# Kernel optimization log

Hardware: AMD Instinct MI355X
Metric: run time of the kernel (lower is better)

## Reference

```python
import jax, jax.numpy as jnp
import numpy as np


def _propagate(x, src, dst, norm, n):
    # PyG propagate with aggr='add': out[dst_e] += norm_e * x[src_e]
    return jax.ops.segment_sum(x[src] * norm[:, None], dst, num_segments=n)


def _dconv(x, w, b, row, col, norm_out, norm_in, n):
    # DConv with K=2: w has shape (2, 2, c_in, c_out)
    # k=0 term: identity for both diffusion directions
    h = x @ w[0, 0] + x @ w[1, 0]
    # k=1 term: 1-hop diffusion, forward edges and flipped edges
    tx_o = _propagate(x, row, col, norm_out, n)  # out-degree normalized walk
    tx_i = _propagate(x, col, row, norm_in, n)   # edge_index.flip([0]) walk
    h = h + tx_o @ w[0, 1] + tx_i @ w[1, 1]
    return h + b


def reference(x, edge_index, edge_weight, w_lin2, b_lin2, w_z, b_z, w_r, b_r, w_h, b_h, w_out, b_out):
    n = x.shape[0]
    row, col = edge_index[0], edge_index[1]
    # degrees from weighted adjacency (same as to_dense_adj row/col sums)
    deg_out = jax.ops.segment_sum(edge_weight, row, num_segments=n)
    deg_in = jax.ops.segment_sum(edge_weight, col, num_segments=n)
    norm_out = (1.0 / deg_out)[row]
    norm_in = (1.0 / deg_in)[row]

    h = x.reshape(n, -1)                      # Flatten: (n, 24)
    h = jax.nn.sigmoid(h @ w_lin2 + b_lin2)   # (n, hidden)

    # DCRNN GRU cell, hidden state initialized to zeros (single step)
    h0 = jnp.zeros_like(h)
    xh = jnp.concatenate([h, h0], axis=1)     # (n, 2*hidden)
    z = jax.nn.sigmoid(_dconv(xh, w_z, b_z, row, col, norm_out, norm_in, n))
    r = jax.nn.sigmoid(_dconv(xh, w_r, b_r, row, col, norm_out, norm_in, n))
    xhr = jnp.concatenate([h, h0 * r], axis=1)
    h_tilde = jnp.tanh(_dconv(xhr, w_h, b_h, row, col, norm_out, norm_in, n))
    h_new = z * h0 + (1.0 - z) * h_tilde

    return jax.nn.sigmoid(h_new) @ w_out + b_out  # (n, out_periods)


def setup_inputs() -> dict:
    key = jax.random.key(0)
    ks = jax.random.split(key, 12)
    N, DEG, HID, OUTP, WIN, HOR = 100000, 8, 64, 12, 2, 12
    E = N * DEG

    x = jax.random.normal(ks[0], (N, WIN, HOR), dtype=jnp.float32)

    # random edges + a ring so every node has out-degree>=1 and in-degree>=1
    e_rand = N * (DEG - 1)
    row_r = jax.random.randint(ks[1], (e_rand,), 0, N, dtype=jnp.int32)
    col_r = jax.random.randint(ks[2], (e_rand,), 0, N, dtype=jnp.int32)
    ring = jnp.arange(N, dtype=jnp.int32)
    row = jnp.concatenate([row_r, ring])
    col = jnp.concatenate([col_r, (ring + 1) % N])
    edge_index = jnp.stack([row, col])  # (2, E)
    edge_weight = jax.random.uniform(ks[3], (E,), minval=0.5, maxval=1.5, dtype=jnp.float32)

    def lin_w(k, fi, fo):
        return jax.random.normal(k, (fi, fo), jnp.float32) / np.float32(np.sqrt(fi))

    def dconv_w(k, cin, cout):
        return jax.random.normal(k, (2, 2, cin, cout), jnp.float32) / np.float32(np.sqrt(cin))

    cin = 2 * HID
    return {
        "x": x,
        "edge_index": edge_index,
        "edge_weight": edge_weight,
        "w_lin2": lin_w(ks[4], WIN * HOR, HID),
        "b_lin2": jnp.zeros((HID,), jnp.float32),
        "w_z": dconv_w(ks[5], cin, HID),
        "b_z": jnp.zeros((HID,), jnp.float32),
        "w_r": dconv_w(ks[6], cin, HID),
        "b_r": jnp.zeros((HID,), jnp.float32),
        "w_h": dconv_w(ks[7], cin, HID),
        "b_h": jnp.zeros((HID,), jnp.float32),
        "w_out": lin_w(ks[8], HID, OUTP),
        "b_out": jnp.zeros((OUTP,), jnp.float32),
    }
```

## Files before the change

### kernel.cpp

```cpp
#include <hip/hip_runtime.h>


typedef unsigned long long ull;
typedef unsigned short ushort;
typedef unsigned int uint;
typedef __attribute__((ext_vector_type(8))) short bf16x8;
typedef __attribute__((ext_vector_type(4))) float f32x4;

#define BSZ    64
#define CAP    768
#define CHUNK  12288
#define MAXBKT 2048

__device__ __forceinline__ float sigmoid_f(float x) {
    return 1.0f / (1.0f + __expf(-x));
}
__device__ __forceinline__ float tanh_f(float x) {
    float ax = fabsf(x);
    float e = __expf(-2.0f * ax);
    float t = (1.0f - e) / (1.0f + e);
    return copysignf(t, x);
}
__device__ __forceinline__ ushort f2bf(float f) {
    unsigned u = __float_as_uint(f);
    return (ushort)((u + 0x7FFF + ((u >> 16) & 1)) >> 16);
}

__global__ void __launch_bounds__(256) mega1_kernel(
        const int* __restrict__ row, const int* __restrict__ col,
        const float* __restrict__ ew, int E,
        uint* __restrict__ gcur, ull* __restrict__ pkbuf,
        int nbkt, int nslot,
        const float* __restrict__ x, const float* __restrict__ Wl,
        const float* __restrict__ bl, ushort* __restrict__ hb, int N,
        const float* __restrict__ wz, const float* __restrict__ bz,
        const float* __restrict__ wh, const float* __restrict__ bh,
        ushort* __restrict__ Wp, float* __restrict__ bc, int SB, int LB) {
    __shared__ float Ws[24 * 64];
    __shared__ float bs[64];
    __shared__ uint hist[MAXBKT];
    __shared__ uint base_s[MAXBKT];
    int bx = blockIdx.x;
    const int t = threadIdx.x;

    if (bx < SB) {
        const int d  = bx & 1;
        const int e0 = (bx >> 1) * CHUNK;
        const int* key = d ? row : col;
        const int* oth = d ? col : row;
        for (int i = t; i < nbkt; i += 256) hist[i] = 0;
        __syncthreads();
#pragma unroll
        for (int j = 0; j < CHUNK / 256; ++j) {
            int e = e0 + j * 256 + t;
            if (e < E) atomicAdd(&hist[key[e] >> 6], 1u);
        }
        __syncthreads();
        for (int i = t; i < nbkt; i += 256) {
            uint c = hist[i];
            base_s[i] = c ? (uint)i * CAP + atomicAdd(&gcur[d * nbkt + i], c) : 0u;
            hist[i] = 0;
        }
        __syncthreads();
#pragma unroll
        for (int j = 0; j < CHUNK / 256; ++j) {
            int e = e0 + j * 256 + t;
            if (e < E) {
                int k   = key[e];
                int bkt = k >> 6;
                uint w15 = (uint)(ew[e] * 16384.0f + 0.5f);
                uint s = base_s[bkt] + atomicAdd(&hist[bkt], 1u);
                if (s < ((uint)bkt + 1u) * CAP)
                    pkbuf[(size_t)d * nslot + s] =
                        ((ull)(uint)oth[e] << 32) |
                        ((uint)(k & (BSZ - 1)) << 15) | w15;
            }
        }
        return;
    }
    bx -= SB;
    if (bx < LB) {
        for (int i = t; i < 384; i += 256)
            ((float4*)Ws)[i] = ((const float4*)Wl)[i];
        if (t < 64) bs[t] = bl[t];
        __syncthreads();
        int gid = bx * 256 + t;
        int n = gid >> 6;
        int c = gid & 63;
        if (n >= N) return;
        const float* xr = x + (size_t)n * 24;
        float acc = bs[c];
#pragma unroll
        for (int k4 = 0; k4 < 6; ++k4) {
            float4 xv = *(const float4*)(xr + k4 * 4);
            acc = fmaf(xv.x, Ws[(k4 * 4 + 0) * 64 + c], acc);
            acc = fmaf(xv.y, Ws[(k4 * 4 + 1) * 64 + c], acc);
            acc = fmaf(xv.z, Ws[(k4 * 4 + 2) * 64 + c], acc);
            acc = fmaf(xv.w, Ws[(k4 * 4 + 3) * 64 + c], acc);
        }
        hb[(size_t)n * 64 + c] = f2bf(sigmoid_f(acc));
        return;
    }
    bx -= LB;
    int i = bx * 256 + t;
    if (bx == 0 && t < 128) bc[t] = (t < 64) ? bz[t] : bh[t - 64];
    if (i >= 6 * 8 * 64 * 8) return;
    int j    = i & 7;
    int lane = (i >> 3) & 63;
    int ct   = (i >> 9) & 7;
    int kt   = i >> 12;
    int k = kt * 32 + 8 * (lane >> 4) + j;
    int c = ct * 16 + (lane & 15);
    const float* w = (c < 64) ? wz : wh;
    int cc = c & 63;
    float v;
    if (k < 64)        v = w[(0 * 128 + k) * 64 + cc] + w[(2 * 128 + k) * 64 + cc];
    else if (k < 128)  v = w[(1 * 128 + (k - 64)) * 64 + cc];
    else               v = w[(3 * 128 + (k - 128)) * 64 + cc];
    Wp[i] = f2bf(v);
}

__global__ void __launch_bounds__(256) sort_kernel(
        const uint* __restrict__ gcur, const ull* __restrict__ pkbuf,
        uint* __restrict__ srt, int2* __restrict__ be,
        float* __restrict__ rdi, float* __restrict__ rdo,
        int nbkt, int nslot, int N) {
    __shared__ uint hist[BSZ];
    __shared__ uint cur[BSZ];
    __shared__ float sdeg[BSZ];
    const int b = blockIdx.x, d = blockIdx.y, t = threadIdx.x;
    if (t < BSZ) { hist[t] = 0; sdeg[t] = 0.0f; }
    __syncthreads();
    uint cnt = gcur[d * nbkt + b];
    if (cnt > CAP) cnt = CAP;
    const ull* rec = pkbuf + (size_t)d * nslot + (size_t)b * CAP;
    for (uint i = t; i < cnt; i += 256) {
        ull r = rec[i];
        uint dl = (uint)(r >> 15) & (BSZ - 1);
        atomicAdd(&hist[dl], 1u);
        atomicAdd(&sdeg[dl], (float)(uint)(r & 0x7FFFu));
    }
    __syncthreads();
    if (t < BSZ) {
        int v = (int)hist[t];
        int x = v;
#pragma unroll
        for (int off = 1; off < BSZ; off <<= 1) {
            int y = __shfl_up(x, off, 64);
            if (t >= off) x += y;
        }
        uint p = (uint)(x - v);
        cur[t] = p;
        int n = b * BSZ + t;
        if (n < N) {
            be[(size_t)d * N + n] =
                make_int2((int)((uint)b * CAP + p),
                          (int)((uint)b * CAP + p + (uint)v));
            float s = sdeg[t];
            float rv = (s > 0.0f) ? (16384.0f / s) : 0.0f;
            if (d == 0) rdi[n] = rv;
            else        rdo[n] = rv;
        }
    }
    __syncthreads();
    uint* so = srt + (size_t)d * nslot + (size_t)b * CAP;
    for (uint i = t; i < cnt; i += 256) {
        ull r = rec[i];
        uint dl = (uint)(r >> 15) & (BSZ - 1);
        uint p = atomicAdd(&cur[dl], 1u);
        so[p] = (uint)(r >> 32);
    }
}

__global__ void __launch_bounds__(256) gather_kernel(
        const ushort* __restrict__ hb, const uint* __restrict__ srt,
        const int2* __restrict__ be,
        const float* __restrict__ rdo, const float* __restrict__ rdi,
        ushort* __restrict__ pob, ushort* __restrict__ pib,
        int nslot, int N) {
    const int lane = threadIdx.x & 63;
    const int g    = lane >> 4;
    const int cq   = (lane & 15) * 4;
    const int d    = blockIdx.y;
    const uint* s_  = srt + (size_t)d * nslot;
    const int2* be_ = be + (size_t)d * N;

    int wid  = blockIdx.x * 4 + (threadIdx.x >> 6);
    int step = gridDim.x * 4;
    if (wid >= N) return;

    int2 r0 = be_[wid];
    uint ia = s_[min(r0.x + g,     r0.y - 1)];
    uint ib = s_[min(r0.x + 4 + g, r0.y - 1)];

    for (int n = wid; n < N; n += step) {
        int nn = n + step;
        bool has_next = (nn < N);
        int2 r1 = r0;
        if (has_next) r1 = be_[nn];

        float a0 = 0.f, a1 = 0.f, a2 = 0.f, a3 = 0.f;
        int s = r0.x, e = r0.y;
        while (s < e) {
            int sn = s + 8;
            uint ia_n = ia, ib_n = ib;
            if (sn < e) {
                ia_n = s_[min(sn + g,     e - 1)];
                ib_n = s_[min(sn + 4 + g, e - 1)];
            } else if (has_next) {
                ia_n = s_[min(r1.x + g,     r1.y - 1)];
                ib_n = s_[min(r1.x + 4 + g, r1.y - 1)];
            }
            bool va = (s + g < e), vb = (s + 4 + g < e);
            float wa, wb;
            if (d == 0) {
                wa = va ? rdo[ia] : 0.0f;
                wb = vb ? rdo[ib] : 0.0f;
            } else {
                wa = va ? 1.0f : 0.0f;
                wb = vb ? 1.0f : 0.0f;
            }
            uint2 ha = *(const uint2*)(hb + (size_t)ia * 64 + cq);
            uint2 hc = *(const uint2*)(hb + (size_t)ib * 64 + cq);
            a0 = fmaf(__uint_as_float(ha.x << 16),         wa, a0);
            a1 = fmaf(__uint_as_float(ha.x & 0xFFFF0000u), wa, a1);
            a2 = fmaf(__uint_as_float(ha.y << 16),         wa, a2);
            a3 = fmaf(__uint_as_float(ha.y & 0xFFFF0000u), wa, a3);
            a0 = fmaf(__uint_as_float(hc.x << 16),         wb, a0);
            a1 = fmaf(__uint_as_float(hc.x & 0xFFFF0000u), wb, a1);
            a2 = fmaf(__uint_as_float(hc.y << 16),         wb, a2);
            a3 = fmaf(__uint_as_float(hc.y & 0xFFFF0000u), wb, a3);
            s = sn; ia = ia_n; ib = ib_n;
        }
        a0 += __shfl_xor(a0, 16, 64); a0 += __shfl_xor(a0, 32, 64);
        a1 += __shfl_xor(a1, 16, 64); a1 += __shfl_xor(a1, 32, 64);
        a2 += __shfl_xor(a2, 16, 64); a2 += __shfl_xor(a2, 32, 64);
        a3 += __shfl_xor(a3, 16, 64); a3 += __shfl_xor(a3, 32, 64);

        if (lane < 16) {
            float m = (d == 0) ? 1.0f : rdi[n];
            uint lo = (uint)f2bf(a0 * m) | ((uint)f2bf(a1 * m) << 16);
            uint hi = (uint)f2bf(a2 * m) | ((uint)f2bf(a3 * m) << 16);
            ushort* dst = (d == 0 ? pob : pib) + (size_t)n * 64 + cq;
            *(uint2*)dst = make_uint2(lo, hi);
        }
        r0 = r1;
    }
}

__global__ void __launch_bounds__(256) gates_kernel(
        const ushort* __restrict__ hb, const ushort* __restrict__ pob,
        const ushort* __restrict__ pib, const ushort* __restrict__ Wp,
        const float* __restrict__ bc, const float* __restrict__ wout,
        const float* __restrict__ bout, float* __restrict__ out, int N) {
    __shared__ float sS[64 * 68];
    __shared__ float sWO[64 * 12];
    const int t    = threadIdx.x;
    const int w    = t >> 6;
    const int lane = t & 63;
    const int n0   = blockIdx.x * 64;

    for (int i = t; i < 64 * 12; i += 256) sWO[i] = wout[i];

    f32x4 acc[8];
#pragma unroll
    for (int ct = 0; ct < 8; ++ct) {
        float bcv = bc[ct * 16 + (lane & 15)];
        acc[ct] = (f32x4){bcv, bcv, bcv, bcv};
    }

    int arow = n0 + w * 16 + (lane & 15);
    if (arow >= N) arow = N - 1;
    const int g8 = (lane >> 4) * 8;
    const ushort* const srcs[3] = {hb, pob, pib};

#pragma unroll
    for (int kc = 0; kc < 6; ++kc) {
        const ushort* src = srcs[kc >> 1];
        bf16x8 a = *(const bf16x8*)(src + (size_t)arow * 64 + (kc & 1) * 32 + g8);
#pragma unroll
        for (int ct = 0; ct < 8; ++ct) {
            bf16x8 b = *(const bf16x8*)(Wp + (size_t)((kc * 8 + ct) * 64 + lane) * 8);
            acc[ct] = __builtin_amdgcn_mfma_f32_16x16x32_bf16(a, b, acc[ct], 0, 0, 0);
        }
    }

    const int rowbase = w * 16 + (lane >> 4) * 4;
    const int colbase = lane & 15;
#pragma unroll
    for (int ct = 0; ct < 4; ++ct) {
#pragma unroll
        for (int r = 0; r < 4; ++r) {
            float zv = sigmoid_f(acc[ct][r]);
            float ht = tanh_f(acc[ct + 4][r]);
            sS[(rowbase + r) * 68 + ct * 16 + colbase] =
                sigmoid_f((1.0f - zv) * ht);
        }
    }
    __syncthreads();

#pragma unroll
    for (int rr = 0; rr < 3; ++rr) {
        int o = rr * 256 + t;
        int node = o / 12;
        int j = o % 12;
        int n = n0 + node;
        if (n >= N) continue;
        float a = bout[j];
#pragma unroll 8
        for (int c2 = 0; c2 < 64; ++c2) a = fmaf(sS[node * 68 + c2], sWO[c2 * 12 + j], a);
        out[(size_t)n * 12 + j] = a;
    }
}

extern "C" void kernel_launch(void* const* d_in, const int* in_sizes, int n_in,
                              void* d_out, int out_size, void* d_ws, size_t ws_size,
                              hipStream_t stream) {
    const float* x      = (const float*)d_in[0];
    const int*   ei     = (const int*)  d_in[1];
    const float* ew     = (const float*)d_in[2];
    const float* w_lin2 = (const float*)d_in[3];
    const float* b_lin2 = (const float*)d_in[4];
    const float* w_z    = (const float*)d_in[5];
    const float* b_z    = (const float*)d_in[6];
    const float* w_h    = (const float*)d_in[9];
    const float* b_h    = (const float*)d_in[10];
    const float* w_out  = (const float*)d_in[11];
    const float* b_out  = (const float*)d_in[12];

    int N = in_sizes[0] / 24;
    int E = in_sizes[1] / 2;
    const int* row = ei;
    const int* col = ei + E;
    int nbkt  = (N + BSZ - 1) / BSZ;
    int nslot = nbkt * CAP;

    ull*    pkbuf = (ull*)d_ws;
    uint*   srt   = (uint*)(pkbuf + 2 * (size_t)nslot);
    ushort* hb    = (ushort*)(srt + 2 * (size_t)nslot);
    ushort* pob   = hb  + (size_t)N * 64;
    ushort* pib   = pob + (size_t)N * 64;
    ushort* Wp    = pib + (size_t)N * 64;
    float*  bc    = (float*)(Wp + 24576);
    float*  rdo   = bc + 128;
    float*  rdi   = rdo + N;
    int2*   be    = (int2*)(rdi + N);
    uint*   gcur  = (uint*)(be + 2 * (size_t)N);

    int SB = 2 * ((E + CHUNK - 1) / CHUNK);
    int LB = (N * 64 + 255) / 256;
    int PB = (6 * 8 * 64 * 8 + 255) / 256;

    hipMemsetAsync(gcur, 0, 2 * (size_t)nbkt * sizeof(uint), stream);
    mega1_kernel<<<SB + LB + PB, 256, 0, stream>>>(
        row, col, ew, E, gcur, pkbuf, nbkt, nslot,
        x, w_lin2, b_lin2, hb, N,
        w_z, b_z, w_h, b_h, Wp, bc, SB, LB);
    sort_kernel<<<dim3(nbkt, 2), 256, 0, stream>>>(gcur, pkbuf, srt, be,
                                                   rdi, rdo, nbkt, nslot, N);
    gather_kernel<<<dim3(2048, 2), 256, 0, stream>>>(hb, srt, be, rdo, rdi,
                                                     pob, pib, nslot, N);
    gates_kernel<<<(N + 63) / 64, 256, 0, stream>>>(hb, pob, pib, Wp, bc,
                                                    w_out, b_out, (float*)d_out, N);
}
```

Baseline: 160.3 us.

## Pack edge bucket records into 32 bits and shrink shared memory use

Each bucketed edge record shrinks from a 64-bit word to a 32-bit word. The neighbor id takes the top 17 bits, the local destination 6 bits and a 9-bit quantized edge weight. This halves the write and read traffic of the bucket buffer between the scatter and sort kernels. The histogram and base-offset shared arrays are merged into one buffer reused by the linear stage, which cuts LDS per block, and the linear stage now has each block handle 16 nodes. The cost is coarser quantization of edge weights in the degree sums, and node ids must fit in 17 bits.

New measurement: 160.1 us. No clear change (-0.1%).

```diff
diff --git a/kernel.cpp b/kernel.cpp
--- a/kernel.cpp
+++ b/kernel.cpp
@@ -29,21 +29,19 @@
 __global__ void __launch_bounds__(256) mega1_kernel(
         const int* __restrict__ row, const int* __restrict__ col,
         const float* __restrict__ ew, int E,
-        uint* __restrict__ gcur, ull* __restrict__ pkbuf,
+        uint* __restrict__ gcur, uint* __restrict__ pkbuf,
         int nbkt, int nslot,
         const float* __restrict__ x, const float* __restrict__ Wl,
         const float* __restrict__ bl, ushort* __restrict__ hb, int N,
         const float* __restrict__ wz, const float* __restrict__ bz,
         const float* __restrict__ wh, const float* __restrict__ bh,
         ushort* __restrict__ Wp, float* __restrict__ bc, int SB, int LB) {
-    __shared__ float Ws[24 * 64];
-    __shared__ float bs[64];
-    __shared__ uint hist[MAXBKT];
-    __shared__ uint base_s[MAXBKT];
+    __shared__ uint smem[MAXBKT];
     int bx = blockIdx.x;
     const int t = threadIdx.x;
 
     if (bx < SB) {
+        uint* hist = smem;
         const int d  = bx & 1;
         const int e0 = (bx >> 1) * CHUNK;
         const int* key = d ? row : col;
@@ -58,8 +56,7 @@
         __syncthreads();
         for (int i = t; i < nbkt; i += 256) {
             uint c = hist[i];
-            base_s[i] = c ? (uint)i * CAP + atomicAdd(&gcur[d * nbkt + i], c) : 0u;
-            hist[i] = 0;
+            hist[i] = c ? (uint)i * CAP + atomicAdd(&gcur[d * nbkt + i], c) : 0u;
         }
         __syncthreads();
 #pragma unroll
@@ -68,37 +65,43 @@
             if (e < E) {
                 int k   = key[e];
                 int bkt = k >> 6;
-                uint w15 = (uint)(ew[e] * 16384.0f + 0.5f);
-                uint s = base_s[bkt] + atomicAdd(&hist[bkt], 1u);
+                uint w9 = (uint)(ew[e] * 256.0f + 0.5f);
+                uint s = atomicAdd(&hist[bkt], 1u);
                 if (s < ((uint)bkt + 1u) * CAP)
                     pkbuf[(size_t)d * nslot + s] =
-                        ((ull)(uint)oth[e] << 32) |
-                        ((uint)(k & (BSZ - 1)) << 15) | w15;
+                        ((uint)oth[e] << 15) |
+                        ((uint)(k & (BSZ - 1)) << 9) | w9;
             }
         }
         return;
     }
     bx -= SB;
     if (bx < LB) {
+        float* Ws = (float*)smem;
+        float* bs = Ws + 24 * 64;
         for (int i = t; i < 384; i += 256)
             ((float4*)Ws)[i] = ((const float4*)Wl)[i];
         if (t < 64) bs[t] = bl[t];
         __syncthreads();
-        int gid = bx * 256 + t;
-        int n = gid >> 6;
-        int c = gid & 63;
-        if (n >= N) return;
-        const float* xr = x + (size_t)n * 24;
-        float acc = bs[c];
-#pragma unroll
-        for (int k4 = 0; k4 < 6; ++k4) {
-            float4 xv = *(const float4*)(xr + k4 * 4);
-            acc = fmaf(xv.x, Ws[(k4 * 4 + 0) * 64 + c], acc);
-            acc = fmaf(xv.y, Ws[(k4 * 4 + 1) * 64 + c], acc);
-            acc = fmaf(xv.z, Ws[(k4 * 4 + 2) * 64 + c], acc);
-            acc = fmaf(xv.w, Ws[(k4 * 4 + 3) * 64 + c], acc);
-        }
-        hb[(size_t)n * 64 + c] = f2bf(sigmoid_f(acc));
+        const int c = t & 63;
+        const int w = t >> 6;
+        const int n0 = bx * 16 + w * 4;
+#pragma unroll
+        for (int q = 0; q < 4; ++q) {
+            int n = n0 + q;
+            if (n >= N) break;
+            const float* xr = x + (size_t)n * 24;
+            float acc = bs[c];
+#pragma unroll
+            for (int k4 = 0; k4 < 6; ++k4) {
+                float4 xv = *(const float4*)(xr + k4 * 4);
+                acc = fmaf(xv.x, Ws[(k4 * 4 + 0) * 64 + c], acc);
+                acc = fmaf(xv.y, Ws[(k4 * 4 + 1) * 64 + c], acc);
+                acc = fmaf(xv.z, Ws[(k4 * 4 + 2) * 64 + c], acc);
+                acc = fmaf(xv.w, Ws[(k4 * 4 + 3) * 64 + c], acc);
+            }
+            hb[(size_t)n * 64 + c] = f2bf(sigmoid_f(acc));
+        }
         return;
     }
     bx -= LB;
@@ -121,7 +124,7 @@
 }
 
 __global__ void __launch_bounds__(256) sort_kernel(
-        const uint* __restrict__ gcur, const ull* __restrict__ pkbuf,
+        const uint* __restrict__ gcur, const uint* __restrict__ pkbuf,
         uint* __restrict__ srt, int2* __restrict__ be,
         float* __restrict__ rdi, float* __restrict__ rdo,
         int nbkt, int nslot, int N) {
@@ -133,12 +136,12 @@
     __syncthreads();
     uint cnt = gcur[d * nbkt + b];
     if (cnt > CAP) cnt = CAP;
-    const ull* rec = pkbuf + (size_t)d * nslot + (size_t)b * CAP;
+    const uint* rec = pkbuf + (size_t)d * nslot + (size_t)b * CAP;
     for (uint i = t; i < cnt; i += 256) {
-        ull r = rec[i];
-        uint dl = (uint)(r >> 15) & (BSZ - 1);
+        uint r = rec[i];
+        uint dl = (r >> 9) & (BSZ - 1);
         atomicAdd(&hist[dl], 1u);
-        atomicAdd(&sdeg[dl], (float)(uint)(r & 0x7FFFu));
+        atomicAdd(&sdeg[dl], (float)(r & 0x1FFu));
     }
     __syncthreads();
     if (t < BSZ) {
@@ -157,7 +160,7 @@
                 make_int2((int)((uint)b * CAP + p),
                           (int)((uint)b * CAP + p + (uint)v));
             float s = sdeg[t];
-            float rv = (s > 0.0f) ? (16384.0f / s) : 0.0f;
+            float rv = (s > 0.0f) ? (256.0f / s) : 0.0f;
             if (d == 0) rdi[n] = rv;
             else        rdo[n] = rv;
         }
@@ -165,10 +168,10 @@
     __syncthreads();
     uint* so = srt + (size_t)d * nslot + (size_t)b * CAP;
     for (uint i = t; i < cnt; i += 256) {
-        ull r = rec[i];
-        uint dl = (uint)(r >> 15) & (BSZ - 1);
+        uint r = rec[i];
+        uint dl = (r >> 9) & (BSZ - 1);
         uint p = atomicAdd(&cur[dl], 1u);
-        so[p] = (uint)(r >> 32);
+        so[p] = r >> 15;
     }
 }
 
@@ -335,8 +338,8 @@
     int nbkt  = (N + BSZ - 1) / BSZ;
     int nslot = nbkt * CAP;
 
-    ull*    pkbuf = (ull*)d_ws;
-    uint*   srt   = (uint*)(pkbuf + 2 * (size_t)nslot);
+    uint*   pkbuf = (uint*)d_ws;
+    uint*   srt   = pkbuf + 2 * (size_t)nslot;
     ushort* hb    = (ushort*)(srt + 2 * (size_t)nslot);
     ushort* pob   = hb  + (size_t)N * 64;
     ushort* pib   = pob + (size_t)N * 64;
@@ -348,7 +351,7 @@
     uint*   gcur  = (uint*)(be + 2 * (size_t)N);
 
     int SB = 2 * ((E + CHUNK - 1) / CHUNK);
-    int LB = (N * 64 + 255) / 256;
+    int LB = (N + 15) / 16;
     int PB = (6 * 8 * 64 * 8 + 255) / 256;
 
     hipMemsetAsync(gcur, 0, 2 * (size_t)nbkt * sizeof(uint), stream);
```
